# Optimization experiments

Hardware: AMD Instinct MI355X
Metric: run time of the kernel (lower is better)

## Reference

```python
import jax, jax.numpy as jnp
import numpy as np

Q = 127.0  # int8 absmax quantization denominator


def _make_quant_weight(key, out_dim, in_dim):
    """Emulate bitsandbytes Linear8bitLt weight: int8 matrix + per-row absmax scale."""
    k1, k2 = jax.random.split(key)
    w_fp = jax.random.normal(k1, (out_dim, in_dim), dtype=jnp.float32) * 0.02
    scale = jnp.max(jnp.abs(w_fp), axis=1)  # [out_dim] per-row absmax
    w_int8 = jnp.clip(jnp.round(w_fp / scale[:, None] * Q), -127, 127).astype(jnp.int8)
    return w_int8, scale


def setup_inputs() -> dict:
    key = jax.random.key(0)
    ks = jax.random.split(key, 4)
    B, S, H, I = 4, 1024, 5120, 12288
    x = jax.random.normal(ks[0], (B, S, H), dtype=jnp.float32)
    w_gate, s_gate = _make_quant_weight(ks[1], I, H)
    w_up, s_up = _make_quant_weight(ks[2], I, H)
    w_down, s_down = _make_quant_weight(ks[3], H, I)
    return {"x": x, "w_gate": w_gate, "s_gate": s_gate,
            "w_up": w_up, "s_up": s_up,
            "w_down": w_down, "s_down": s_down}


def _qlinear(x, w_int8, scale):
    # y = x @ dequant(W)^T ; dequant(W) = w_int8 * scale/127 per output row.
    # Fold scale after the matmul (equivalent, avoids materializing dequant W twice).
    y = jnp.einsum("bsh,oh->bso", x, w_int8.astype(x.dtype))
    return y * (scale / Q)


def reference(x, w_gate, s_gate, w_up, s_up, w_down, s_down):
    gate = jax.nn.silu(_qlinear(x, w_gate, s_gate))  # [B,S,I]
    up = _qlinear(x, w_up, s_up)                     # [B,S,I]
    return _qlinear(gate * up, w_down, s_down)       # [B,S,H]
```

## Files before the change

### kernel.cpp

```cpp
#include <hip/hip_runtime.h>
#include <hip/hip_bf16.h>
#include <stdint.h>

typedef unsigned short u16;
typedef __attribute__((ext_vector_type(4))) float floatx4;
typedef __attribute__((ext_vector_type(8))) short bf16x8;
typedef __attribute__((ext_vector_type(8))) unsigned short u16x8;
typedef const __attribute__((address_space(1))) void gvoid;
typedef __attribute__((address_space(3))) void lvoid;

static constexpr int Mdim = 4096;
static constexpr int Hdim = 5120;
static constexpr int Idim = 12288;
static constexpr float QINV = 1.0f / 127.0f;

static __device__ __forceinline__ u16 f2b(float f) {
    __hip_bfloat16 h = __float2bfloat16(f);
    return *(u16*)&h;
}

__global__ void conv_i32_to_bf16(const int* __restrict__ in, u16* __restrict__ out) {
    int idx = (blockIdx.x * 256 + threadIdx.x) * 8;
    int4 v0 = *(const int4*)(in + idx);
    int4 v1 = *(const int4*)(in + idx + 4);
    u16x8 o;
    o[0] = f2b((float)v0.x); o[1] = f2b((float)v0.y);
    o[2] = f2b((float)v0.z); o[3] = f2b((float)v0.w);
    o[4] = f2b((float)v1.x); o[5] = f2b((float)v1.y);
    o[6] = f2b((float)v1.z); o[7] = f2b((float)v1.w);
    *(u16x8*)(out + idx) = o;
}

__global__ void conv_f32_to_bf16(const float* __restrict__ in, u16* __restrict__ out) {
    int idx = (blockIdx.x * 256 + threadIdx.x) * 8;
    float4 v0 = *(const float4*)(in + idx);
    float4 v1 = *(const float4*)(in + idx + 4);
    u16x8 o;
    o[0] = f2b(v0.x); o[1] = f2b(v0.y); o[2] = f2b(v0.z); o[3] = f2b(v0.w);
    o[4] = f2b(v1.x); o[5] = f2b(v1.y); o[6] = f2b(v1.z); o[7] = f2b(v1.w);
    *(u16x8*)(out + idx) = o;
}

template<int MODE>
__global__ __launch_bounds__(512, 2)
void gemm256(const u16* __restrict__ A, const u16* __restrict__ Bw,
             const float* __restrict__ scale, u16* __restrict__ GateBuf,
             float* __restrict__ OutF, int N, int K, int nbx)
{
    __shared__ u16 As[4 * 8192];
    __shared__ u16 Bs[4 * 8192];

    const int tid  = threadIdx.x;
    const int lane = tid & 63;
    const int wave = tid >> 6;
    const int wm = (wave >> 2) * 128;
    const int wn = (wave & 3) * 64;
    const int lm = lane & 15;
    const int lg = lane >> 4;

    const int nwg = gridDim.x;
    const int bid = blockIdx.x;
    const int swz = (bid & 7) * (nwg >> 3) + (bid >> 3);
    const int row0 = (swz % nbx) * 256;
    const int col0 = (swz / nbx) * 256;

    const u16* Ablk = A  + (size_t)row0 * K;
    const u16* Bblk = Bw + (size_t)col0 * K;

    const int rs  = tid >> 2;
    const int csw = ((tid & 3) ^ ((rs >> 1) & 3)) << 3;
    const u16* aS = Ablk + (size_t)rs * K + csw;
    const u16* bS = Bblk + (size_t)rs * K + csw;
    const size_t rK128 = (size_t)128 * K;
    u16* aD = As + tid * 8;
    u16* bD = Bs + tid * 8;

    const int koff = (lg ^ ((lm >> 1) & 3)) << 3;

    floatx4 acc[8][4];
    #pragma unroll
    for (int i = 0; i < 8; i++)
        #pragma unroll
        for (int j = 0; j < 4; j++)
            acc[i][j] = (floatx4){0.f, 0.f, 0.f, 0.f};

    const int nt = K >> 5;

#define STAGE_A(t) do { \
    const u16* s_ = aS + (size_t)(t) * 32; \
    u16* d_ = aD + ((t) & 3) * 8192; \
    __builtin_amdgcn_global_load_lds((gvoid*)s_, (lvoid*)d_, 16, 0, 0); \
    __builtin_amdgcn_global_load_lds((gvoid*)(s_ + rK128), (lvoid*)(d_ + 4096), 16, 0, 0); \
} while (0)

#define STAGE_B(t) do { \
    const u16* s_ = bS + (size_t)(t) * 32; \
    u16* d_ = bD + ((t) & 3) * 8192; \
    __builtin_amdgcn_global_load_lds((gvoid*)s_, (lvoid*)d_, 16, 0, 0); \
    __builtin_amdgcn_global_load_lds((gvoid*)(s_ + rK128), (lvoid*)(d_ + 4096), 16, 0, 0); \
} while (0)

#define PHASE(qr, STG, WAITV) do { \
    bf16x8 af[4], bf[4]; \
    const u16* Ab_ = As + bufo; \
    const u16* Bb_ = Bs + bufo; \
    _Pragma("unroll") \
    for (int i = 0; i < 4; i++) \
        af[i] = *(const bf16x8*)(Ab_ + (wm + ((qr) * 4 + i) * 16 + lm) * 32 + koff); \
    _Pragma("unroll") \
    for (int j = 0; j < 4; j++) \
        bf[j] = *(const bf16x8*)(Bb_ + (wn + j * 16 + lm) * 32 + koff); \
    STG; \
    asm volatile("" ::: "memory"); \
    __builtin_amdgcn_s_barrier(); \
    __builtin_amdgcn_s_setprio(1); \
    _Pragma("unroll") \
    for (int i = 0; i < 4; i++) \
        _Pragma("unroll") \
        for (int j = 0; j < 4; j++) \
            acc[(qr) * 4 + i][j] = __builtin_amdgcn_mfma_f32_16x16x32_bf16( \
                af[i], bf[j], acc[(qr) * 4 + i][j], 0, 0, 0); \
    __builtin_amdgcn_s_setprio(0); \
    WAITV; \
    asm volatile("" ::: "memory"); \
    __builtin_amdgcn_s_barrier(); \
} while (0)

    STAGE_A(0); STAGE_B(0);
    STAGE_A(1); STAGE_B(1);
    STAGE_A(2); STAGE_B(2);
    asm volatile("s_waitcnt vmcnt(8)" ::: "memory");
    __builtin_amdgcn_s_barrier();

    int t = 0;
    for (; t < nt - 3; ++t) {
        const int bufo = (t & 3) * 8192;
        PHASE(0, STAGE_A(t + 3), (void)0);
        PHASE(1, STAGE_B(t + 3), asm volatile("s_waitcnt vmcnt(8)" ::: "memory"));
    }
    {
        const int bufo = (t & 3) * 8192;
        PHASE(0, (void)0, (void)0);
        PHASE(1, (void)0, asm volatile("s_waitcnt vmcnt(4)" ::: "memory"));
        ++t;
    }
    {
        const int bufo = (t & 3) * 8192;
        PHASE(0, (void)0, (void)0);
        PHASE(1, (void)0, asm volatile("s_waitcnt vmcnt(0)" ::: "memory"));
        ++t;
    }
    {
        const int bufo = (t & 3) * 8192;
        PHASE(0, (void)0, (void)0);
        PHASE(1, (void)0, (void)0);
    }
#undef PHASE
#undef STAGE_A
#undef STAGE_B

    const int ln = lane & 15;
    const int rq = (lane >> 4) * 4;
    #pragma unroll
    for (int j = 0; j < 4; j++) {
        const int col = col0 + wn + j * 16 + ln;
        const float s = scale[col] * QINV;
        #pragma unroll
        for (int i = 0; i < 8; i++) {
            const int rowb = row0 + wm + i * 16 + rq;
            #pragma unroll
            for (int r = 0; r < 4; r++) {
                const size_t idx = (size_t)(rowb + r) * N + col;
                float v = acc[i][j][r] * s;
                if (MODE == 0) {
                    float g = v / (1.0f + __expf(-v));
                    GateBuf[idx] = f2b(g);
                } else if (MODE == 1) {
                    u16 gu = GateBuf[idx];
                    float g = __bfloat162float(*(__hip_bfloat16*)&gu);
                    GateBuf[idx] = f2b(g * v);
                } else {
                    OutF[idx] = v;
                }
            }
        }
    }
}

extern "C" void kernel_launch(void* const* d_in, const int* in_sizes, int n_in,
                              void* d_out, int out_size, void* d_ws, size_t ws_size,
                              hipStream_t stream)
{
    const float* x  = (const float*)d_in[0];
    const int*   wg = (const int*)d_in[1];
    const float* sg = (const float*)d_in[2];
    const int*   wu = (const int*)d_in[3];
    const float* su = (const float*)d_in[4];
    const int*   wd = (const int*)d_in[5];
    const float* sd = (const float*)d_in[6];
    float* out = (float*)d_out;

    char* ws = (char*)d_ws;
    u16* xb   = (u16*)ws;
    u16* wb   = (u16*)(ws + 41943040);
    u16* gate = (u16*)(ws + 41943040 + 125829120);

    conv_f32_to_bf16<<<10240, 256, 0, stream>>>(x, xb);

    conv_i32_to_bf16<<<30720, 256, 0, stream>>>(wg, wb);
    gemm256<0><<<(Mdim / 256) * (Idim / 256), 512, 0, stream>>>(
        xb, wb, sg, gate, nullptr, Idim, Hdim, Mdim / 256);

    conv_i32_to_bf16<<<30720, 256, 0, stream>>>(wu, wb);
    gemm256<1><<<(Mdim / 256) * (Idim / 256), 512, 0, stream>>>(
        xb, wb, su, gate, nullptr, Idim, Hdim, Mdim / 256);

    conv_i32_to_bf16<<<30720, 256, 0, stream>>>(wd, wb);
    gemm256<2><<<(Mdim / 256) * (Hdim / 256), 512, 0, stream>>>(
        gate, wb, sd, nullptr, out, Hdim, Idim, Mdim / 256);
}
```

Before: 2.581 ms.

## Restructure GEMM main loop to one barrier per k-tile

Replaces the two-phase loop, which split A and B staging across half-tiles and used four workgroup barriers per k-tile, with a simpler schedule. Each iteration now waits for the current tile, does one barrier, issues all global-to-LDS loads for tile t+3, then runs all MFMAs for tile t. The B fragments are loaded once per tile and the A fragments in two halves. The aim is to cut barrier and synchronisation overhead. In exchange, load issue is no longer interleaved between compute phases, and the wave-priority handling changes.

```diff
diff --git a/kernel.cpp b/kernel.cpp
--- a/kernel.cpp
+++ b/kernel.cpp
@@ -86,78 +86,66 @@
 
     const int nt = K >> 5;
 
-#define STAGE_A(t) do { \
-    const u16* s_ = aS + (size_t)(t) * 32; \
-    u16* d_ = aD + ((t) & 3) * 8192; \
-    __builtin_amdgcn_global_load_lds((gvoid*)s_, (lvoid*)d_, 16, 0, 0); \
-    __builtin_amdgcn_global_load_lds((gvoid*)(s_ + rK128), (lvoid*)(d_ + 4096), 16, 0, 0); \
+#define STAGE(t) do { \
+    const u16* sA_ = aS + (size_t)(t) * 32; \
+    const u16* sB_ = bS + (size_t)(t) * 32; \
+    u16* dA_ = aD + ((t) & 3) * 8192; \
+    u16* dB_ = bD + ((t) & 3) * 8192; \
+    __builtin_amdgcn_global_load_lds((gvoid*)sA_, (lvoid*)dA_, 16, 0, 0); \
+    __builtin_amdgcn_global_load_lds((gvoid*)(sA_ + rK128), (lvoid*)(dA_ + 4096), 16, 0, 0); \
+    __builtin_amdgcn_global_load_lds((gvoid*)sB_, (lvoid*)dB_, 16, 0, 0); \
+    __builtin_amdgcn_global_load_lds((gvoid*)(sB_ + rK128), (lvoid*)(dB_ + 4096), 16, 0, 0); \
 } while (0)
 
-#define STAGE_B(t) do { \
-    const u16* s_ = bS + (size_t)(t) * 32; \
-    u16* d_ = bD + ((t) & 3) * 8192; \
-    __builtin_amdgcn_global_load_lds((gvoid*)s_, (lvoid*)d_, 16, 0, 0); \
-    __builtin_amdgcn_global_load_lds((gvoid*)(s_ + rK128), (lvoid*)(d_ + 4096), 16, 0, 0); \
-} while (0)
-
-#define PHASE(qr, STG, WAITV) do { \
-    bf16x8 af[4], bf[4]; \
+#define COMPUTE(t) do { \
+    const int bufo = ((t) & 3) * 8192; \
     const u16* Ab_ = As + bufo; \
     const u16* Bb_ = Bs + bufo; \
-    _Pragma("unroll") \
-    for (int i = 0; i < 4; i++) \
-        af[i] = *(const bf16x8*)(Ab_ + (wm + ((qr) * 4 + i) * 16 + lm) * 32 + koff); \
+    bf16x8 bf[4]; \
     _Pragma("unroll") \
     for (int j = 0; j < 4; j++) \
         bf[j] = *(const bf16x8*)(Bb_ + (wn + j * 16 + lm) * 32 + koff); \
-    STG; \
-    asm volatile("" ::: "memory"); \
-    __builtin_amdgcn_s_barrier(); \
-    __builtin_amdgcn_s_setprio(1); \
     _Pragma("unroll") \
-    for (int i = 0; i < 4; i++) \
+    for (int q = 0; q < 2; q++) { \
+        bf16x8 af[4]; \
         _Pragma("unroll") \
-        for (int j = 0; j < 4; j++) \
-            acc[(qr) * 4 + i][j] = __builtin_amdgcn_mfma_f32_16x16x32_bf16( \
-                af[i], bf[j], acc[(qr) * 4 + i][j], 0, 0, 0); \
-    __builtin_amdgcn_s_setprio(0); \
-    WAITV; \
-    asm volatile("" ::: "memory"); \
-    __builtin_amdgcn_s_barrier(); \
+        for (int i = 0; i < 4; i++) \
+            af[i] = *(const bf16x8*)(Ab_ + (wm + (q * 4 + i) * 16 + lm) * 32 + koff); \
+        __builtin_amdgcn_s_setprio(1); \
+        _Pragma("unroll") \
+        for (int i = 0; i < 4; i++) \
+            _Pragma("unroll") \
+            for (int j = 0; j < 4; j++) \
+                acc[q * 4 + i][j] = __builtin_amdgcn_mfma_f32_16x16x32_bf16( \
+                    af[i], bf[j], acc[q * 4 + i][j], 0, 0, 0); \
+        __builtin_amdgcn_s_setprio(0); \
+    } \
 } while (0)
 
-    STAGE_A(0); STAGE_B(0);
-    STAGE_A(1); STAGE_B(1);
-    STAGE_A(2); STAGE_B(2);
+    STAGE(0); STAGE(1); STAGE(2);
+
+    int t = 0;
+    for (; t < nt - 3; ++t) {
+        asm volatile("s_waitcnt vmcnt(8)" ::: "memory");
+        __builtin_amdgcn_s_barrier();
+        asm volatile("" ::: "memory");
+        STAGE(t + 3);
+        COMPUTE(t);
+    }
     asm volatile("s_waitcnt vmcnt(8)" ::: "memory");
     __builtin_amdgcn_s_barrier();
-
-    int t = 0;
-    for (; t < nt - 3; ++t) {
-        const int bufo = (t & 3) * 8192;
-        PHASE(0, STAGE_A(t + 3), (void)0);
-        PHASE(1, STAGE_B(t + 3), asm volatile("s_waitcnt vmcnt(8)" ::: "memory"));
-    }
-    {
-        const int bufo = (t & 3) * 8192;
-        PHASE(0, (void)0, (void)0);
-        PHASE(1, (void)0, asm volatile("s_waitcnt vmcnt(4)" ::: "memory"));
-        ++t;
-    }
-    {
-        const int bufo = (t & 3) * 8192;
-        PHASE(0, (void)0, (void)0);
-        PHASE(1, (void)0, asm volatile("s_waitcnt vmcnt(0)" ::: "memory"));
-        ++t;
-    }
-    {
-        const int bufo = (t & 3) * 8192;
-        PHASE(0, (void)0, (void)0);
-        PHASE(1, (void)0, (void)0);
-    }
-#undef PHASE
-#undef STAGE_A
-#undef STAGE_B
+    asm volatile("" ::: "memory");
+    COMPUTE(nt - 3);
+    asm volatile("s_waitcnt vmcnt(4)" ::: "memory");
+    __builtin_amdgcn_s_barrier();
+    asm volatile("" ::: "memory");
+    COMPUTE(nt - 2);
+    asm volatile("s_waitcnt vmcnt(0)" ::: "memory");
+    __builtin_amdgcn_s_barrier();
+    asm volatile("" ::: "memory");
+    COMPUTE(nt - 1);
+#undef COMPUTE
+#undef STAGE
 
     const int ln = lane & 15;
     const int rq = (lane >> 4) * 4;
```

New measurement: 3.073 ms. +19.1%, slower.
